# Performance work log

Measured on AMD Instinct MI355X. Metric: run time of the kernel, lower is better.

Reference implementation:

```python
import jax, jax.numpy as jnp
import numpy as np
from math import sqrt

P_DROP = 0.2  # dropout_rate

def setup_inputs() -> dict:
    key = jax.random.key(0)
    ks = jax.random.split(key, 5)
    B, Cin, H, W = 32, 128, 64, 64
    Cout, kh, kw = 256, 3, 3
    k = sqrt(1.0 / (Cin * kh * kw))  # He-style init std from module
    x = jax.random.normal(ks[0], (B, Cin, H, W), dtype=jnp.float32)
    weight = jax.random.normal(ks[1], (Cout, Cin, kh, kw), dtype=jnp.float32) * k
    bias = jax.random.normal(ks[2], (Cout,), dtype=jnp.float32) * k
    # uniforms used for torch.rand(...) > p per batch element ('w' mode draws fresh masks per sample)
    u_w = jax.random.uniform(ks[3], (B, Cout, Cin, kh, kw), dtype=jnp.float32)
    u_b = jax.random.uniform(ks[4], (B, Cout), dtype=jnp.float32)
    return {"x": x, "weight": weight, "bias": bias, "u_w": u_w, "u_b": u_b}

def reference(x, weight, bias, u_w, u_b):
    # 'w' mode: per-sample dropped-out weight/bias, conv per sample -> vmapped batched conv.
    # Note: mask is (rand > p) with NO 1/(1-p) rescaling, matching the torch code.
    w_mask = (u_w > P_DROP).astype(weight.dtype)          # [B,O,I,kh,kw]
    b_mask = (u_b > P_DROP).astype(bias.dtype)            # [B,O]
    w_per = weight[None] * w_mask                          # [B,O,I,kh,kw]
    b_per = bias[None] * b_mask                            # [B,O]

    def conv_one(xi, wi):  # xi: [Cin,H,W], wi: [O,I,kh,kw]
        return jax.lax.conv_general_dilated(
            xi[None], wi,
            window_strides=(1, 1),
            padding=((1, 1), (1, 1)),
            dimension_numbers=("NCHW", "OIHW", "NCHW"),
        )[0]

    y = jax.vmap(conv_one)(x, w_per)                       # [B,O,H,W]
    return y + b_per[:, :, None, None]
```

## Files before the change

kernel.cpp:

```cpp
#include <hip/hip_runtime.h>
#include <cstdint>
#include <cstddef>

#define CIN   128
#define COUT  256
#define HW    64
#define NSP   4096
#define KTOT  1152
#define BATCH 32
#define PDROP 0.2f
#define LDT   40

__device__ __forceinline__ unsigned short f2bf(float f) {
    unsigned int u = __builtin_bit_cast(unsigned int, f);
    u += 0x7fffu + ((u >> 16) & 1u);
    return (unsigned short)(u >> 16);
}

__device__ __align__(16) unsigned short g_zeros[64] = {0};

__device__ __forceinline__ void gl_lds16(const unsigned short* g, unsigned short* l) {
    __builtin_amdgcn_global_load_lds(
        (const __attribute__((address_space(1))) unsigned int*)g,
        (__attribute__((address_space(3))) unsigned int*)l,
        16, 0, 0);
}

__global__ __launch_bounds__(128) void mask_weights(
        const float* __restrict__ weight, const float* __restrict__ u_w,
        unsigned short* __restrict__ wt)
{
    __shared__ unsigned short tile[KTOT];
    const int bo = blockIdx.x;
    const int o  = bo & (COUT - 1);
    const int t  = threadIdx.x;
    const float4* wsrc = reinterpret_cast<const float4*>(weight + (size_t)o  * KTOT);
    const float4* usrc = reinterpret_cast<const float4*>(u_w    + (size_t)bo * KTOT);
    #pragma unroll
    for (int j = 0; j < 3; ++j) {
        const int idx = j * 128 + t;
        if (idx < KTOT / 4) {
            float4 wv = wsrc[idx];
            float4 uv = usrc[idx];
            const float w4[4] = {wv.x, wv.y, wv.z, wv.w};
            const float u4[4] = {uv.x, uv.y, uv.z, uv.w};
            #pragma unroll
            for (int c = 0; c < 4; ++c) {
                const int ks = idx * 4 + c;
                const int i  = ks / 9;
                const int r  = ks - 9 * i;
                tile[r * CIN + i] = f2bf((u4[c] > PDROP) ? w4[c] : 0.f);
            }
        }
    }
    __syncthreads();
    const uint4* src = reinterpret_cast<const uint4*>(tile);
    uint4* dst = reinterpret_cast<uint4*>(wt + (size_t)bo * KTOT);
    #pragma unroll
    for (int j = 0; j < 2; ++j) {
        const int idx = j * 128 + t;
        if (idx < KTOT / 8) dst[idx] = src[idx];
    }
}

__global__ __launch_bounds__(256) void transpose_x(
        const float* __restrict__ x, unsigned short* __restrict__ xt)
{
    __shared__ unsigned short tile[64 * 136];
    const int b   = blockIdx.y;
    const int hw0 = blockIdx.x * 64;
    const int t   = threadIdx.x;
    const int ib  = t >> 4;
    const int hw4 = (t & 15) * 4;
    #pragma unroll
    for (int j = 0; j < 8; ++j) {
        const int i = ib + 16 * j;
        const float4 v = *reinterpret_cast<const float4*>(
            x + ((size_t)(b * CIN + i)) * NSP + hw0 + hw4);
        const float v4[4] = {v.x, v.y, v.z, v.w};
        #pragma unroll
        for (int c = 0; c < 4; ++c)
            tile[(hw4 + c) * 136 + i] = f2bf(v4[c]);
    }
    __syncthreads();
    #pragma unroll
    for (int j = 0; j < 4; ++j) {
        const int idx  = j * 256 + t;
        const int row  = idx >> 4;
        const int part = idx & 15;
        const uint4 v = *reinterpret_cast<const uint4*>(&tile[row * 136 + part * 8]);
        *reinterpret_cast<uint4*>(
            xt + ((size_t)(b * NSP + hw0 + row)) * CIN + part * 8) = v;
    }
}

__global__ __launch_bounds__(256) void conv_v3(
        const unsigned short* __restrict__ wt,
        const unsigned short* __restrict__ xt,
        const float* __restrict__ bias, const float* __restrict__ u_b,
        float* __restrict__ out)
{
    using frag  = __attribute__((ext_vector_type(8))) short;
    using f32x4 = __attribute__((ext_vector_type(4))) float;

    __shared__ unsigned short As[128 * 64];
    __shared__ unsigned short Bs[128 * 64];

    const int tid  = threadIdx.x;
    const int lane = tid & 63;
    const int q    = lane >> 4;
    const int l15  = lane & 15;
    const int wv   = tid >> 6;
    const int wm   = (wv >> 1) * 64;
    const int wn   = (wv & 1) * 64;

    const int b  = blockIdx.z;
    const int m0 = blockIdx.y * 128;
    const int n0 = blockIdx.x * 128;

    const int r8 = lane >> 3;
    const int p8 = lane & 7;
    const int cx = p8 ^ r8;

    const unsigned short* wtb = wt + (size_t)(b * COUT + m0) * KTOT;
    const unsigned short* xtb = xt + (size_t)b * NSP * CIN;

    const unsigned short* gA[4];
    int py[4], px[4];
    #pragma unroll
    for (int j = 0; j < 4; ++j) {
        const int row = wv * 32 + j * 8 + r8;
        gA[j] = wtb + (size_t)row * KTOT + cx * 8;
        const int p_sp = n0 + row;
        py[j] = p_sp >> 6;
        px[j] = p_sp & 63;
    }
    unsigned short* ldsA[4];
    unsigned short* ldsB[4];
    #pragma unroll
    for (int j = 0; j < 4; ++j) {
        ldsA[j] = &As[(wv * 32 + j * 8) * 64];
        ldsB[j] = &Bs[(wv * 32 + j * 8) * 64];
    }

    f32x4 acc[4][4];
    #pragma unroll
    for (int i = 0; i < 4; ++i)
        #pragma unroll
        for (int j = 0; j < 4; ++j)
            acc[i][j] = (f32x4){0.f, 0.f, 0.f, 0.f};

    const int l7 = l15 & 7;
    const int physk0 = (q)     ^ l7;
    const int physk1 = (4 + q) ^ l7;
    const int a_base = (wm + l15) * 64;
    const int b_base = (wn + l15) * 64;

    for (int s = 0; s < 18; ++s) {
        const int r  = s >> 1;
        const int i0 = (s & 1) * 64;
        const int dy = r / 3 - 1;
        const int dx = r - 3 * (r / 3) - 1;

        __syncthreads();

        #pragma unroll
        for (int j = 0; j < 4; ++j) {
            gl_lds16(gA[j], ldsA[j]);
            gA[j] += 64;
            const int hh = py[j] + dy;
            const int ww = px[j] + dx;
            const bool valid = ((unsigned)hh < 64u) && ((unsigned)ww < 64u);
            const unsigned short* srcB = valid
                ? xtb + (size_t)(hh * HW + ww) * CIN + i0 + cx * 8
                : g_zeros + p8 * 8;
            gl_lds16(srcB, ldsB[j]);
        }

        __syncthreads();

        #pragma unroll
        for (int ki = 0; ki < 2; ++ki) {
            const int pk = ki ? physk1 : physk0;
            frag af[4], bfr[4];
            #pragma unroll
            for (int mi = 0; mi < 4; ++mi)
                af[mi] = *reinterpret_cast<const frag*>(
                    &As[a_base + mi * 1024 + pk * 8]);
            #pragma unroll
            for (int ni = 0; ni < 4; ++ni)
                bfr[ni] = *reinterpret_cast<const frag*>(
                    &Bs[b_base + ni * 1024 + pk * 8]);
            #pragma unroll
            for (int mi = 0; mi < 4; ++mi)
                #pragma unroll
                for (int ni = 0; ni < 4; ++ni)
                    acc[mi][ni] = __builtin_amdgcn_mfma_f32_16x16x32_bf16(
                        af[mi], bfr[ni], acc[mi][ni], 0, 0, 0);
        }
    }

    float* ob = out + (size_t)b * COUT * NSP;
    #pragma unroll
    for (int mi = 0; mi < 4; ++mi) {
        #pragma unroll
        for (int rg = 0; rg < 4; ++rg) {
            const int o  = m0 + wm + mi * 16 + q * 4 + rg;
            const float bvv = (u_b[b * COUT + o] > PDROP) ? bias[o] : 0.f;
            float* orow = ob + (size_t)o * NSP + n0 + wn + l15;
            #pragma unroll
            for (int ni = 0; ni < 4; ++ni)
                orow[ni * 16] = acc[mi][ni][rg] + bvv;
        }
    }
}

template<bool USE_WS>
__global__ __launch_bounds__(256) void conv_fb(
        const float* __restrict__ x, const float* __restrict__ weight,
        const float* __restrict__ bias, const float* __restrict__ u_w,
        const float* __restrict__ u_b, const unsigned short* __restrict__ wt,
        float* __restrict__ out)
{
    using frag  = __attribute__((ext_vector_type(8))) short;
    using f32x4 = __attribute__((ext_vector_type(4))) float;

    __shared__ unsigned short As[128 * LDT];
    __shared__ unsigned short Bs[128 * LDT];

    const int tid  = threadIdx.x;
    const int lane = tid & 63;
    const int q    = lane >> 4;
    const int l15  = lane & 15;
    const int wv   = tid >> 6;
    const int wm   = (wv >> 1) * 64;
    const int wn   = (wv & 1) * 64;

    const int b  = blockIdx.z;
    const int m0 = blockIdx.y * 128;
    const int n0 = blockIdx.x * 128;

    const int arow = tid >> 1;
    const int acol = (tid & 1) * 16;
    const int pn = tid & 127;
    const int kh = (tid >> 7) * 16;
    const int p  = n0 + pn;
    const int ph = p >> 6;
    const int pw = p & 63;

    const float* xb = x + (size_t)b * CIN * NSP;

    f32x4 acc[4][4];
    #pragma unroll
    for (int i = 0; i < 4; ++i)
        #pragma unroll
        for (int j = 0; j < 4; ++j)
            acc[i][j] = (f32x4){0.f, 0.f, 0.f, 0.f};

    const int a_rd = (wm + l15) * LDT + q * 8;
    const int b_rd = (wn + l15) * LDT + q * 8;

    for (int s = 0; s < 36; ++s) {
        const int r  = s >> 2;
        const int i0 = (s & 3) * 32;
        const int k0 = s * 32;

        uint4 av0, av1;
        float aw[16], au[16];
        if (USE_WS) {
            const uint4* src = reinterpret_cast<const uint4*>(
                wt + ((size_t)(b * COUT + m0 + arow)) * KTOT + k0 + acol);
            av0 = src[0];
            av1 = src[1];
        } else {
            const float* wsrc = weight + (size_t)(m0 + arow) * KTOT;
            const float* usrc = u_w + (size_t)(b * COUT + m0 + arow) * KTOT;
            #pragma unroll
            for (int ii = 0; ii < 16; ++ii) {
                const int kk = (i0 + acol + ii) * 9 + r;
                aw[ii] = wsrc[kk];
                au[ii] = usrc[kk];
            }
        }

        const int hh = ph + (r / 3) - 1;
        const int ww = pw + (r % 3) - 1;
        float bx[16];
        #pragma unroll
        for (int j = 0; j < 16; ++j) bx[j] = 0.f;
        if (((unsigned)hh < 64u) && ((unsigned)ww < 64u)) {
            const float* xsrc = xb + (size_t)(i0 + kh) * NSP + hh * HW + ww;
            #pragma unroll
            for (int j = 0; j < 16; ++j) bx[j] = xsrc[(size_t)j * NSP];
        }

        __syncthreads();

        if (USE_WS) {
            uint4* d = reinterpret_cast<uint4*>(&As[arow * LDT + acol]);
            d[0] = av0; d[1] = av1;
        } else {
            union { unsigned short u16[16]; uint4 v[2]; } tu;
            #pragma unroll
            for (int ii = 0; ii < 16; ++ii)
                tu.u16[ii] = f2bf((au[ii] > PDROP) ? aw[ii] : 0.f);
            uint4* d = reinterpret_cast<uint4*>(&As[arow * LDT + acol]);
            d[0] = tu.v[0]; d[1] = tu.v[1];
        }
        {
            union { unsigned short u16[16]; uint4 v[2]; } tu;
            #pragma unroll
            for (int j = 0; j < 16; ++j) tu.u16[j] = f2bf(bx[j]);
            uint4* d = reinterpret_cast<uint4*>(&Bs[pn * LDT + kh]);
            d[0] = tu.v[0]; d[1] = tu.v[1];
        }

        __syncthreads();

        frag af[4], bfr[4];
        #pragma unroll
        for (int mi = 0; mi < 4; ++mi)
            af[mi] = *reinterpret_cast<const frag*>(&As[a_rd + mi * 16 * LDT]);
        #pragma unroll
        for (int ni = 0; ni < 4; ++ni)
            bfr[ni] = *reinterpret_cast<const frag*>(&Bs[b_rd + ni * 16 * LDT]);
        #pragma unroll
        for (int mi = 0; mi < 4; ++mi)
            #pragma unroll
            for (int ni = 0; ni < 4; ++ni)
                acc[mi][ni] = __builtin_amdgcn_mfma_f32_16x16x32_bf16(
                    af[mi], bfr[ni], acc[mi][ni], 0, 0, 0);
    }

    float* ob = out + (size_t)b * COUT * NSP;
    #pragma unroll
    for (int mi = 0; mi < 4; ++mi) {
        #pragma unroll
        for (int rg = 0; rg < 4; ++rg) {
            const int o = m0 + wm + mi * 16 + q * 4 + rg;
            const float bvv = (u_b[b * COUT + o] > PDROP) ? bias[o] : 0.f;
            float* orow = ob + (size_t)o * NSP + n0 + wn + l15;
            #pragma unroll
            for (int ni = 0; ni < 4; ++ni)
                orow[ni * 16] = acc[mi][ni][rg] + bvv;
        }
    }
}

extern "C" void kernel_launch(void* const* d_in, const int* in_sizes, int n_in,
                              void* d_out, int out_size, void* d_ws, size_t ws_size,
                              hipStream_t stream)
{
    const float* x      = (const float*)d_in[0];
    const float* weight = (const float*)d_in[1];
    const float* bias   = (const float*)d_in[2];
    const float* u_w    = (const float*)d_in[3];
    const float* u_b    = (const float*)d_in[4];
    float* out = (float*)d_out;

    const size_t wt_bytes = (size_t)BATCH * COUT * KTOT * sizeof(unsigned short);
    const size_t xt_bytes = (size_t)BATCH * NSP * CIN * sizeof(unsigned short);
    dim3 grid(NSP / 128, COUT / 128, BATCH);

    if (ws_size >= wt_bytes + xt_bytes) {
        unsigned short* wtp = (unsigned short*)d_ws;
        unsigned short* xtp = (unsigned short*)((char*)d_ws + wt_bytes);
        mask_weights<<<BATCH * COUT, 128, 0, stream>>>(weight, u_w, wtp);
        transpose_x<<<dim3(NSP / 64, BATCH), 256, 0, stream>>>(x, xtp);
        conv_v3<<<grid, 256, 0, stream>>>(wtp, xtp, bias, u_b, out);
    } else if (ws_size >= wt_bytes) {
        unsigned short* wtp = (unsigned short*)d_ws;
        mask_weights<<<BATCH * COUT, 128, 0, stream>>>(weight, u_w, wtp);
        conv_fb<true><<<grid, 256, 0, stream>>>(x, weight, bias, u_w, u_b, wtp, out);
    } else {
        conv_fb<false><<<grid, 256, 0, stream>>>(x, weight, bias, u_w, u_b, nullptr, out);
    }
}
```

Measured before the change: 319.2 us.

## Stage padded input rows in LDS once per channel half, merge prepass kernels

The conv kernel now loads a 4-row haloed tile of input (two image rows plus borders) into LDS once per 64-channel half and reuses it across all nine taps through shifted offsets. Before, it regathered im2col B tiles from global memory for every tap. The weight masking and input transposition kernels are merged into one launch, and the conv gets a launch_bounds occupancy hint of 3. This cuts global and L2 traffic and removes one launch, at the cost of more LDS per block and a more complex swizzle for the halo.

Result: faster. 284.1 us (-11.0%).

```diff
diff --git a/kernel.cpp b/kernel.cpp
--- a/kernel.cpp
+++ b/kernel.cpp
@@ -26,75 +26,77 @@
         16, 0, 0);
 }
 
-__global__ __launch_bounds__(128) void mask_weights(
+__global__ __launch_bounds__(256) void prepass(
         const float* __restrict__ weight, const float* __restrict__ u_w,
-        unsigned short* __restrict__ wt)
+        const float* __restrict__ x,
+        unsigned short* __restrict__ wt, unsigned short* __restrict__ xt)
 {
-    __shared__ unsigned short tile[KTOT];
-    const int bo = blockIdx.x;
-    const int o  = bo & (COUT - 1);
-    const int t  = threadIdx.x;
-    const float4* wsrc = reinterpret_cast<const float4*>(weight + (size_t)o  * KTOT);
-    const float4* usrc = reinterpret_cast<const float4*>(u_w    + (size_t)bo * KTOT);
-    #pragma unroll
-    for (int j = 0; j < 3; ++j) {
-        const int idx = j * 128 + t;
-        if (idx < KTOT / 4) {
-            float4 wv = wsrc[idx];
-            float4 uv = usrc[idx];
-            const float w4[4] = {wv.x, wv.y, wv.z, wv.w};
-            const float u4[4] = {uv.x, uv.y, uv.z, uv.w};
-            #pragma unroll
-            for (int c = 0; c < 4; ++c) {
-                const int ks = idx * 4 + c;
-                const int i  = ks / 9;
-                const int r  = ks - 9 * i;
-                tile[r * CIN + i] = f2bf((u4[c] > PDROP) ? w4[c] : 0.f);
+    __shared__ unsigned short sh[8704];
+    const int t256 = threadIdx.x;
+
+    if (blockIdx.x < 4096) {
+        const int half = t256 >> 7;
+        const int t    = t256 & 127;
+        const int bo   = blockIdx.x * 2 + half;
+        const int o    = bo & (COUT - 1);
+        unsigned short* tile = sh + half * KTOT;
+        const float4* wsrc = reinterpret_cast<const float4*>(weight + (size_t)o  * KTOT);
+        const float4* usrc = reinterpret_cast<const float4*>(u_w    + (size_t)bo * KTOT);
+        #pragma unroll
+        for (int j = 0; j < 3; ++j) {
+            const int idx = j * 128 + t;
+            if (idx < KTOT / 4) {
+                float4 wv = wsrc[idx];
+                float4 uv = usrc[idx];
+                const float w4[4] = {wv.x, wv.y, wv.z, wv.w};
+                const float u4[4] = {uv.x, uv.y, uv.z, uv.w};
+                #pragma unroll
+                for (int c = 0; c < 4; ++c) {
+                    const int ks = idx * 4 + c;
+                    const int i  = ks / 9;
+                    const int r  = ks - 9 * i;
+                    tile[r * CIN + i] = f2bf((u4[c] > PDROP) ? w4[c] : 0.f);
+                }
             }
         }
-    }
-    __syncthreads();
-    const uint4* src = reinterpret_cast<const uint4*>(tile);
-    uint4* dst = reinterpret_cast<uint4*>(wt + (size_t)bo * KTOT);
-    #pragma unroll
-    for (int j = 0; j < 2; ++j) {
-        const int idx = j * 128 + t;
-        if (idx < KTOT / 8) dst[idx] = src[idx];
-    }
-}
-
-__global__ __launch_bounds__(256) void transpose_x(
-        const float* __restrict__ x, unsigned short* __restrict__ xt)
-{
-    __shared__ unsigned short tile[64 * 136];
-    const int b   = blockIdx.y;
-    const int hw0 = blockIdx.x * 64;
-    const int t   = threadIdx.x;
-    const int ib  = t >> 4;
-    const int hw4 = (t & 15) * 4;
-    #pragma unroll
-    for (int j = 0; j < 8; ++j) {
-        const int i = ib + 16 * j;
-        const float4 v = *reinterpret_cast<const float4*>(
-            x + ((size_t)(b * CIN + i)) * NSP + hw0 + hw4);
-        const float v4[4] = {v.x, v.y, v.z, v.w};
-        #pragma unroll
-        for (int c = 0; c < 4; ++c)
-            tile[(hw4 + c) * 136 + i] = f2bf(v4[c]);
-    }
-    __syncthreads();
-    #pragma unroll
-    for (int j = 0; j < 4; ++j) {
-        const int idx  = j * 256 + t;
-        const int row  = idx >> 4;
-        const int part = idx & 15;
-        const uint4 v = *reinterpret_cast<const uint4*>(&tile[row * 136 + part * 8]);
-        *reinterpret_cast<uint4*>(
-            xt + ((size_t)(b * NSP + hw0 + row)) * CIN + part * 8) = v;
-    }
-}
-
-__global__ __launch_bounds__(256) void conv_v3(
+        __syncthreads();
+        const uint4* src = reinterpret_cast<const uint4*>(tile);
+        uint4* dst = reinterpret_cast<uint4*>(wt + (size_t)bo * KTOT);
+        #pragma unroll
+        for (int j = 0; j < 2; ++j) {
+            const int idx = j * 128 + t;
+            if (idx < KTOT / 8) dst[idx] = src[idx];
+        }
+    } else {
+        const int bidx = blockIdx.x - 4096;
+        const int b    = bidx >> 6;
+        const int hw0  = (bidx & 63) * 64;
+        const int ib   = t256 >> 4;
+        const int hw4  = (t256 & 15) * 4;
+        #pragma unroll
+        for (int j = 0; j < 8; ++j) {
+            const int i = ib + 16 * j;
+            const float4 v = *reinterpret_cast<const float4*>(
+                x + ((size_t)(b * CIN + i)) * NSP + hw0 + hw4);
+            const float v4[4] = {v.x, v.y, v.z, v.w};
+            #pragma unroll
+            for (int c = 0; c < 4; ++c)
+                sh[(hw4 + c) * 136 + i] = f2bf(v4[c]);
+        }
+        __syncthreads();
+        #pragma unroll
+        for (int j = 0; j < 4; ++j) {
+            const int idx  = j * 256 + t256;
+            const int row  = idx >> 4;
+            const int part = idx & 15;
+            const uint4 v = *reinterpret_cast<const uint4*>(&sh[row * 136 + part * 8]);
+            *reinterpret_cast<uint4*>(
+                xt + ((size_t)(b * NSP + hw0 + row)) * CIN + part * 8) = v;
+        }
+    }
+}
+
+__global__ __launch_bounds__(256, 3) void conv_v4(
         const unsigned short* __restrict__ wt,
         const unsigned short* __restrict__ xt,
         const float* __restrict__ bias, const float* __restrict__ u_b,
@@ -103,8 +105,8 @@
     using frag  = __attribute__((ext_vector_type(8))) short;
     using f32x4 = __attribute__((ext_vector_type(4))) float;
 
+    __shared__ unsigned short Xs[4 * 66 * 64];
     __shared__ unsigned short As[128 * 64];
-    __shared__ unsigned short Bs[128 * 64];
 
     const int tid  = threadIdx.x;
     const int lane = tid & 63;
@@ -113,35 +115,47 @@
     const int wv   = tid >> 6;
     const int wm   = (wv >> 1) * 64;
     const int wn   = (wv & 1) * 64;
-
-    const int b  = blockIdx.z;
-    const int m0 = blockIdx.y * 128;
-    const int n0 = blockIdx.x * 128;
+    const int wnrow = wn >> 6;
+
+    const int b   = blockIdx.z;
+    const int m0  = blockIdx.y * 128;
+    const int n0  = blockIdx.x * 128;
+    const int ph0 = n0 >> 6;
+
+    const unsigned short* wtb = wt + (size_t)(b * COUT + m0) * KTOT;
+    const unsigned short* xtb = xt + (size_t)b * NSP * CIN;
 
     const int r8 = lane >> 3;
     const int p8 = lane & 7;
     const int cx = p8 ^ r8;
-
-    const unsigned short* wtb = wt + (size_t)(b * COUT + m0) * KTOT;
-    const unsigned short* xtb = xt + (size_t)b * NSP * CIN;
-
     const unsigned short* gA[4];
-    int py[4], px[4];
+    unsigned short* ldsA[4];
     #pragma unroll
     for (int j = 0; j < 4; ++j) {
         const int row = wv * 32 + j * 8 + r8;
-        gA[j] = wtb + (size_t)row * KTOT + cx * 8;
-        const int p_sp = n0 + row;
-        py[j] = p_sp >> 6;
-        px[j] = p_sp & 63;
-    }
-    unsigned short* ldsA[4];
-    unsigned short* ldsB[4];
-    #pragma unroll
-    for (int j = 0; j < 4; ++j) {
+        gA[j]   = wtb + (size_t)row * KTOT + cx * 8;
         ldsA[j] = &As[(wv * 32 + j * 8) * 64];
-        ldsB[j] = &Bs[(wv * 32 + j * 8) * 64];
-    }
+    }
+
+    const int kcl = (lane & 7) ^ ((1 + (lane >> 3)) & 7);
+    const int xsrc_lane = (lane >> 3) * CIN + kcl * 8;
+    const int hhx = ph0 - 1 + wv;
+    const bool vrow = ((unsigned)hhx < 64u);
+    unsigned short* const xdst = &Xs[(wv * 66 + 1) * 64];
+
+    const int l7 = l15 & 7;
+    const int physk0 = q ^ l7;
+    const int physk1 = (4 + q) ^ l7;
+    const int a_base = (wm + l15) * 64;
+    int xoff[4];
+    #pragma unroll
+    for (int ni = 0; ni < 4; ++ni) xoff[ni] = (ni * 16 + l15 + 1) * 64;
+    int xr[3][2];
+    #pragma unroll
+    for (int dxi = 0; dxi < 3; ++dxi)
+        #pragma unroll
+        for (int ki = 0; ki < 2; ++ki)
+            xr[dxi][ki] = ((ki * 4 + q) ^ ((l15 + dxi) & 7)) * 8;
 
     f32x4 acc[4][4];
     #pragma unroll
@@ -150,53 +164,65 @@
         for (int j = 0; j < 4; ++j)
             acc[i][j] = (f32x4){0.f, 0.f, 0.f, 0.f};
 
-    const int l7 = l15 & 7;
-    const int physk0 = (q)     ^ l7;
-    const int physk1 = (4 + q) ^ l7;
-    const int a_base = (wm + l15) * 64;
-    const int b_base = (wn + l15) * 64;
-
-    for (int s = 0; s < 18; ++s) {
-        const int r  = s >> 1;
-        const int i0 = (s & 1) * 64;
-        const int dy = r / 3 - 1;
-        const int dx = r - 3 * (r / 3) - 1;
+    {
+        const int cell = tid >> 5;
+        const int rr   = cell >> 1;
+        const int cc   = (cell & 1) ? 65 : 0;
+        *reinterpret_cast<unsigned int*>(
+            &Xs[(rr * 66 + cc) * 64 + (tid & 31) * 2]) = 0u;
+    }
+
+    #pragma unroll
+    for (int s2 = 0; s2 < 2; ++s2) {
+        const int i0 = s2 * 64;
 
         __syncthreads();
 
-        #pragma unroll
-        for (int j = 0; j < 4; ++j) {
-            gl_lds16(gA[j], ldsA[j]);
-            gA[j] += 64;
-            const int hh = py[j] + dy;
-            const int ww = px[j] + dx;
-            const bool valid = ((unsigned)hh < 64u) && ((unsigned)ww < 64u);
-            const unsigned short* srcB = valid
-                ? xtb + (size_t)(hh * HW + ww) * CIN + i0 + cx * 8
-                : g_zeros + p8 * 8;
-            gl_lds16(srcB, ldsB[j]);
-        }
-
-        __syncthreads();
-
-        #pragma unroll
-        for (int ki = 0; ki < 2; ++ki) {
-            const int pk = ki ? physk1 : physk0;
-            frag af[4], bfr[4];
-            #pragma unroll
-            for (int mi = 0; mi < 4; ++mi)
-                af[mi] = *reinterpret_cast<const frag*>(
-                    &As[a_base + mi * 1024 + pk * 8]);
-            #pragma unroll
-            for (int ni = 0; ni < 4; ++ni)
-                bfr[ni] = *reinterpret_cast<const frag*>(
-                    &Bs[b_base + ni * 1024 + pk * 8]);
-            #pragma unroll
-            for (int mi = 0; mi < 4; ++mi)
+        {
+            const unsigned short* sx = vrow
+                ? xtb + (size_t)hhx * HW * CIN + i0 + xsrc_lane
+                : g_zeros;
+            #pragma unroll
+            for (int g = 0; g < 8; ++g)
+                gl_lds16(vrow ? (sx + g * 8 * CIN) : sx, xdst + g * 512);
+        }
+
+        #pragma unroll
+        for (int tap = 0; tap < 9; ++tap) {
+            const int dy  = tap / 3 - 1;
+            const int dx  = tap - 3 * (tap / 3) - 1;
+            const int dxi = dx + 1;
+
+            if (tap) __syncthreads();
+
+            const int k0 = tap * 128 + i0;
+            #pragma unroll
+            for (int j = 0; j < 4; ++j)
+                gl_lds16(gA[j] + k0, ldsA[j]);
+
+            __syncthreads();
+
+            const int cb = (wnrow + dy + 1) * 4224 + dx * 64;
+
+            #pragma unroll
+            for (int ki = 0; ki < 2; ++ki) {
+                const int pk = ki ? physk1 : physk0;
+                frag af[4], bfr[4];
+                #pragma unroll
+                for (int mi = 0; mi < 4; ++mi)
+                    af[mi] = *reinterpret_cast<const frag*>(
+                        &As[a_base + mi * 1024 + pk * 8]);
                 #pragma unroll
                 for (int ni = 0; ni < 4; ++ni)
-                    acc[mi][ni] = __builtin_amdgcn_mfma_f32_16x16x32_bf16(
-                        af[mi], bfr[ni], acc[mi][ni], 0, 0, 0);
+                    bfr[ni] = *reinterpret_cast<const frag*>(
+                        &Xs[cb + xoff[ni] + xr[dxi][ki]]);
+                #pragma unroll
+                for (int mi = 0; mi < 4; ++mi)
+                    #pragma unroll
+                    for (int ni = 0; ni < 4; ++ni)
+                        acc[mi][ni] = __builtin_amdgcn_mfma_f32_16x16x32_bf16(
+                            af[mi], bfr[ni], acc[mi][ni], 0, 0, 0);
+            }
         }
     }
 
@@ -365,12 +391,11 @@
     if (ws_size >= wt_bytes + xt_bytes) {
         unsigned short* wtp = (unsigned short*)d_ws;
         unsigned short* xtp = (unsigned short*)((char*)d_ws + wt_bytes);
-        mask_weights<<<BATCH * COUT, 128, 0, stream>>>(weight, u_w, wtp);
-        transpose_x<<<dim3(NSP / 64, BATCH), 256, 0, stream>>>(x, xtp);
-        conv_v3<<<grid, 256, 0, stream>>>(wtp, xtp, bias, u_b, out);
+        prepass<<<4096 + 2048, 256, 0, stream>>>(weight, u_w, x, wtp, xtp);
+        conv_v4<<<grid, 256, 0, stream>>>(wtp, xtp, bias, u_b, out);
     } else if (ws_size >= wt_bytes) {
         unsigned short* wtp = (unsigned short*)d_ws;
-        mask_weights<<<BATCH * COUT, 128, 0, stream>>>(weight, u_w, wtp);
+        prepass<<<4096, 256, 0, stream>>>(weight, u_w, x, wtp, nullptr);
         conv_fb<true><<<grid, 256, 0, stream>>>(x, weight, bias, u_w, u_b, wtp, out);
     } else {
         conv_fb<false><<<grid, 256, 0, stream>>>(x, weight, bias, u_w, u_b, nullptr, out);
```
